# Kernel tuning notes

Measured on AMD Instinct MI355X. Metric: run time of the kernel, lower is better.

## Reference

```python
import jax, jax.numpy as jnp
import numpy as np

WS = 7           # window size (square)
N = WS * WS      # tokens per window = 49
DIM = 384
HEADS = 12
HEAD_DIM = DIM // HEADS
TABLE = (2 * WS - 1) * (2 * WS - 1)  # 169


def _relative_position_index():
    # Static Swin-style relative position index, shape [N, N], values in [0, TABLE)
    coords = np.stack(np.meshgrid(np.arange(WS), np.arange(WS), indexing='ij'))  # [2, WS, WS]
    flat = coords.reshape(2, -1)                           # [2, N]
    rel = flat[:, :, None] - flat[:, None, :]              # [2, N, N]
    rel = rel.transpose(1, 2, 0)                           # [N, N, 2]
    rel[:, :, 0] += WS - 1
    rel[:, :, 1] += WS - 1
    rel[:, :, 0] *= 2 * WS - 1
    return rel.sum(-1)                                     # [N, N]


REL_IDX = jnp.asarray(_relative_position_index())


def setup_inputs() -> dict:
    key = jax.random.key(0)
    ks = jax.random.split(key, 9)
    B_ = 4096
    return {
        'x_edge': jax.random.normal(ks[0], (B_, N, DIM), jnp.float32),
        'x_body': jax.random.normal(ks[1], (B_, N, DIM), jnp.float32),
        'q_w': jax.random.normal(ks[2], (DIM, DIM), jnp.float32) * 0.02,
        'q_b': jnp.zeros((DIM,), jnp.float32),
        'kv_w': jax.random.normal(ks[3], (DIM, 2 * DIM), jnp.float32) * 0.02,
        'kv_b': jnp.zeros((2 * DIM,), jnp.float32),
        'proj_w': jax.random.normal(ks[4], (DIM, DIM), jnp.float32) * 0.02,
        'proj_b': jnp.zeros((DIM,), jnp.float32),
        'bias_table': jax.random.normal(ks[5], (TABLE, HEADS), jnp.float32) * 0.02,
    }


def reference(x_edge, x_body, q_w, q_b, kv_w, kv_b, proj_w, proj_b, bias_table):
    B_, n, C = x_body.shape
    scale = HEAD_DIM ** -0.5
    # projections
    q = (x_edge @ q_w + q_b).reshape(B_, n, HEADS, HEAD_DIM)           # [B,N,H,d]
    kv = (x_body @ kv_w + kv_b).reshape(B_, n, 2, HEADS, HEAD_DIM)
    k = kv[:, :, 0]                                                     # [B,N,H,d]
    v = kv[:, :, 1]
    # windowed attention scores [B,H,N,N]
    attn = jnp.einsum('bnhd,bmhd->bhnm', q * scale, k)
    # gathered relative position bias [H,N,N]
    bias = bias_table[REL_IDX.reshape(-1)].reshape(n, n, HEADS).transpose(2, 0, 1)
    attn = jax.nn.softmax(attn + bias[None], axis=-1)
    out = jnp.einsum('bhnm,bmhd->bnhd', attn, v).reshape(B_, n, C)
    return out @ proj_w + proj_b
```

## Files before the change

kernel.cpp:

```cpp
#include <hip/hip_runtime.h>
#include <hip/hip_bf16.h>

#define NTOK 49
#define DIM 384
#define HEADS 12
#define SCALE 0.17677669529663687f

typedef __attribute__((ext_vector_type(8))) short bf16x8;
typedef __attribute__((ext_vector_type(4))) float f32x4;

#define MFMA16(a, b, c) __builtin_amdgcn_mfma_f32_16x16x32_bf16((a), (b), (c), 0, 0, 0)

__device__ __forceinline__ short f2bf(float f) {
  __hip_bfloat16 h = __float2bfloat16(f);
  return __builtin_bit_cast(short, h);
}

__device__ __forceinline__ bf16x8 pack8(f32x4 a, f32x4 b) {
  bf16x8 r;
#pragma unroll
  for (int i = 0; i < 4; ++i) { r[i] = f2bf(a[i]); r[i + 4] = f2bf(b[i]); }
  return r;
}

#define WQT_OFF   0
#define WKVT_OFF  147456
#define WPT_OFF   442368
#define BIAS_BYTE_OFF 1179648
#define BIAS_ITEMS (12 * 4 * 4 * 64 * 4)

__global__ void prep_kernel(const float* __restrict__ qw, const float* __restrict__ kvw,
                            const float* __restrict__ pw, const float* __restrict__ bt,
                            short* __restrict__ wsS, float* __restrict__ biasf) {
  int id = blockIdx.x * 256 + threadIdx.x;
  const int SZ1 = 384 * 384;
  const int SZ2 = 768 * 384;
  const int SZ3 = 384 * 384;
  if (id < SZ1) {
    int n = id / 384, k = id % 384;
    wsS[WQT_OFF + id] = f2bf(qw[k * 384 + n]);
  } else if (id < SZ1 + SZ2) {
    int t = id - SZ1; int n = t / 384, k = t % 384;
    wsS[WKVT_OFF + t] = f2bf(kvw[k * 768 + n]);
  } else if (id < SZ1 + SZ2 + SZ3) {
    int t = id - (SZ1 + SZ2); int n = t / 384, k = t % 384;
    wsS[WPT_OFF + t] = f2bf(pw[k * 384 + n]);
  } else if (id < SZ1 + SZ2 + SZ3 + BIAS_ITEMS) {
    int t = id - (SZ1 + SZ2 + SZ3);
    int i  = t & 3;
    int lm = (t >> 2) & 63;
    int tb = (t >> 8) & 3;
    int qt = (t >> 10) & 3;
    int h  = t >> 12;
    int q = qt * 16 + (lm & 15);
    int k = tb * 16 + (lm >> 4) * 4 + i;
    float v = 0.0f;
    if (q < NTOK && k < NTOK) {
      int idx = ((q / 7 - k / 7) + 6) * 13 + ((q % 7 - k % 7) + 6);
      v = bt[idx * HEADS + h];
    }
    biasf[t] = v;
  }
}

#define LDS_ELEMS 38416
#define LDS_BYTES (LDS_ELEMS * 2)

__global__ __launch_bounds__(256, 2)
void fused_kernel(const float* __restrict__ xe, const float* __restrict__ xb,
                  const float* __restrict__ qb, const float* __restrict__ kvb,
                  const float* __restrict__ pb,
                  const short* __restrict__ wqT, const short* __restrict__ wkvT,
                  const short* __restrict__ wpT, const float* __restrict__ biasf,
                  float* __restrict__ out) {
  extern __shared__ short lds[];
  short* X    = lds;
  short* XE   = lds + 19208;
  short* OALL = XE;

  const int b   = blockIdx.x;
  const int tid = threadIdx.x;
  const int u   = tid >> 6;
  const int l   = tid & 63;
  const int m16 = l & 15;
  const int g   = l >> 4;

  const f32x4 zf = {0.f, 0.f, 0.f, 0.f};

  const float* xew = xe + (size_t)b * (NTOK * DIM);
  const float* xbw = xb + (size_t)b * (NTOK * DIM);
  for (int i4 = tid; i4 < 2 * 4704; i4 += 256) {
    int eb = i4 < 4704;
    int e = (eb ? i4 : i4 - 4704) * 4;
    const float* src = eb ? xew : xbw;
    short* dst = eb ? XE : X;
    int r = e / DIM, c = e % DIM;
    float4 v = *(const float4*)(src + e);
    ushort4 s;
    s.x = (unsigned short)f2bf(v.x); s.y = (unsigned short)f2bf(v.y);
    s.z = (unsigned short)f2bf(v.z); s.w = (unsigned short)f2bf(v.w);
    *(ushort4*)&dst[r * 392 + c] = s;
  }
  __syncthreads();

  bf16x8 ofr[3][4];

#pragma unroll
  for (int hh = 0; hh < 3; ++hh) {
    const int h = u * 3 + hh;

    f32x4 qc0[4], qc1[4], kc0[4], kc1[4], vc0[4], vc1[4];
#pragma unroll
    for (int tb = 0; tb < 4; ++tb) {
      qc0[tb] = zf; qc1[tb] = zf; kc0[tb] = zf;
      kc1[tb] = zf; vc0[tb] = zf; vc1[tb] = zf;
    }
    const short* wq0 = wqT  + (size_t)(h * 32 + m16) * 384;
    const short* wq1 = wqT  + (size_t)(h * 32 + 16 + m16) * 384;
    const short* wk0 = wkvT + (size_t)(h * 32 + m16) * 384;
    const short* wk1 = wkvT + (size_t)(h * 32 + 16 + m16) * 384;
    const short* wv0 = wkvT + (size_t)(384 + h * 32 + m16) * 384;
    const short* wv1 = wkvT + (size_t)(384 + h * 32 + 16 + m16) * 384;
    bf16x8 qA0 = *(const bf16x8*)(wq0 + g * 8), qA1 = *(const bf16x8*)(wq1 + g * 8);
    bf16x8 kA0 = *(const bf16x8*)(wk0 + g * 8), kA1 = *(const bf16x8*)(wk1 + g * 8);
    bf16x8 vA0 = *(const bf16x8*)(wv0 + g * 8), vA1 = *(const bf16x8*)(wv1 + g * 8);
#pragma unroll 1
    for (int kk = 0; kk < 12; kk += 2) {
      const int koB = (kk + 1) * 32 + g * 8;
      bf16x8 qB0 = *(const bf16x8*)(wq0 + koB), qB1 = *(const bf16x8*)(wq1 + koB);
      bf16x8 kB0 = *(const bf16x8*)(wk0 + koB), kB1 = *(const bf16x8*)(wk1 + koB);
      bf16x8 vB0 = *(const bf16x8*)(wv0 + koB), vB1 = *(const bf16x8*)(wv1 + koB);
      {
        const int ko = kk * 32 + g * 8;
#pragma unroll
        for (int tb = 0; tb < 4; ++tb) {
          int tr = tb * 16 + m16; tr = tr < 49 ? tr : 48;
          bf16x8 xev = *(const bf16x8*)(&XE[tr * 392 + ko]);
          bf16x8 xbv = *(const bf16x8*)(&X[tr * 392 + ko]);
          qc0[tb] = MFMA16(qA0, xev, qc0[tb]);
          qc1[tb] = MFMA16(qA1, xev, qc1[tb]);
          kc0[tb] = MFMA16(kA0, xbv, kc0[tb]);
          kc1[tb] = MFMA16(kA1, xbv, kc1[tb]);
          vc0[tb] = MFMA16(xbv, vA0, vc0[tb]);
          vc1[tb] = MFMA16(xbv, vA1, vc1[tb]);
        }
      }
      const int koA = ((kk + 2) % 12) * 32 + g * 8;
      qA0 = *(const bf16x8*)(wq0 + koA); qA1 = *(const bf16x8*)(wq1 + koA);
      kA0 = *(const bf16x8*)(wk0 + koA); kA1 = *(const bf16x8*)(wk1 + koA);
      vA0 = *(const bf16x8*)(wv0 + koA); vA1 = *(const bf16x8*)(wv1 + koA);
      {
#pragma unroll
        for (int tb = 0; tb < 4; ++tb) {
          int tr = tb * 16 + m16; tr = tr < 49 ? tr : 48;
          bf16x8 xev = *(const bf16x8*)(&XE[tr * 392 + koB]);
          bf16x8 xbv = *(const bf16x8*)(&X[tr * 392 + koB]);
          qc0[tb] = MFMA16(qB0, xev, qc0[tb]);
          qc1[tb] = MFMA16(qB1, xev, qc1[tb]);
          kc0[tb] = MFMA16(kB0, xbv, kc0[tb]);
          kc1[tb] = MFMA16(kB1, xbv, kc1[tb]);
          vc0[tb] = MFMA16(xbv, vB0, vc0[tb]);
          vc1[tb] = MFMA16(xbv, vB1, vc1[tb]);
        }
      }
    }
    bf16x8 qfr[4], kfr[4], vfr[2][2];
    {
      float4 t0 = *(const float4*)(qb + h * 32 + g * 4);
      float4 t1 = *(const float4*)(qb + h * 32 + 16 + g * 4);
      f32x4 b0 = {t0.x, t0.y, t0.z, t0.w};
      f32x4 b1 = {t1.x, t1.y, t1.z, t1.w};
#pragma unroll
      for (int qt = 0; qt < 4; ++qt)
        qfr[qt] = pack8((qc0[qt] + b0) * SCALE, (qc1[qt] + b1) * SCALE);
    }
    {
      float4 t0 = *(const float4*)(kvb + h * 32 + g * 4);
      float4 t1 = *(const float4*)(kvb + h * 32 + 16 + g * 4);
      f32x4 b0 = {t0.x, t0.y, t0.z, t0.w};
      f32x4 b1 = {t1.x, t1.y, t1.z, t1.w};
#pragma unroll
      for (int tb = 0; tb < 4; ++tb) kfr[tb] = pack8(kc0[tb] + b0, kc1[tb] + b1);
    }
    {
      float vb0 = kvb[384 + h * 32 + m16];
      float vb1 = kvb[384 + h * 32 + 16 + m16];
      f32x4 bv0 = {vb0, vb0, vb0, vb0};
      f32x4 bv1 = {vb1, vb1, vb1, vb1};
#pragma unroll
      for (int t = 0; t < 2; ++t) {
        vfr[t][0] = pack8(vc0[2 * t] + bv0, vc0[2 * t + 1] + bv0);
        vfr[t][1] = pack8(vc1[2 * t] + bv1, vc1[2 * t + 1] + bv1);
      }
    }

    const float4* bfh = (const float4*)biasf + (size_t)h * 4 * 4 * 64;
#pragma unroll
    for (int qt = 0; qt < 4; ++qt) {
      const float4* bq = bfh + qt * 4 * 64;
      float4 c0 = bq[l], c1 = bq[64 + l], c2 = bq[128 + l], c3 = bq[192 + l];
      f32x4 B0 = {c0.x, c0.y, c0.z, c0.w};
      f32x4 B1 = {c1.x, c1.y, c1.z, c1.w};
      f32x4 B2 = {c2.x, c2.y, c2.z, c2.w};
      f32x4 B3 = {c3.x, c3.y, c3.z, c3.w};
      f32x4 s[4];
#pragma unroll
      for (int tb = 0; tb < 4; ++tb) s[tb] = MFMA16(kfr[tb], qfr[qt], zf);

      float sv[4][4];
#pragma unroll
      for (int i = 0; i < 4; ++i) {
        sv[0][i] = s[0][i] + B0[i];
        sv[1][i] = s[1][i] + B1[i];
        sv[2][i] = s[2][i] + B2[i];
        sv[3][i] = (g == 0 && i == 0) ? s[3][0] + B3[0] : -3.0e38f;
      }
      float mx = -3.0e38f;
#pragma unroll
      for (int tb = 0; tb < 4; ++tb)
#pragma unroll
        for (int i = 0; i < 4; ++i) mx = fmaxf(mx, sv[tb][i]);
      mx = fmaxf(mx, __shfl_xor(mx, 16));
      mx = fmaxf(mx, __shfl_xor(mx, 32));
      float sum = 0.f;
#pragma unroll
      for (int tb = 0; tb < 4; ++tb)
#pragma unroll
        for (int i = 0; i < 4; ++i) {
          float e = __expf(sv[tb][i] - mx);
          sv[tb][i] = e;
          sum += e;
        }
      sum += __shfl_xor(sum, 16);
      sum += __shfl_xor(sum, 32);
      float inv = 1.0f / sum;

      bf16x8 pfr[2];
#pragma unroll
      for (int t = 0; t < 2; ++t) {
        f32x4 lo = {sv[2 * t][0] * inv, sv[2 * t][1] * inv, sv[2 * t][2] * inv, sv[2 * t][3] * inv};
        f32x4 hi = {sv[2 * t + 1][0] * inv, sv[2 * t + 1][1] * inv, sv[2 * t + 1][2] * inv, sv[2 * t + 1][3] * inv};
        pfr[t] = pack8(lo, hi);
      }
      f32x4 o0 = zf, o1 = zf;
      o0 = MFMA16(pfr[0], vfr[0][0], o0); o0 = MFMA16(pfr[1], vfr[1][0], o0);
      o1 = MFMA16(pfr[0], vfr[0][1], o1); o1 = MFMA16(pfr[1], vfr[1][1], o1);
      ofr[hh][qt] = pack8(o0, o1);
    }
  }
  __syncthreads();

#pragma unroll
  for (int hh = 0; hh < 3; ++hh) {
    const int h = u * 3 + hh;
#pragma unroll
    for (int qt = 0; qt < 4; ++qt)
#pragma unroll
      for (int i = 0; i < 4; ++i) {
        int r = qt * 16 + g * 4 + i;
        if (r < 49) {
          OALL[r * 392 + h * 32 + m16]      = ofr[hh][qt][i];
          OALL[r * 392 + h * 32 + 16 + m16] = ofr[hh][qt][4 + i];
        }
      }
  }
  __syncthreads();

  {
    f32x4 pacc[4][6];
#pragma unroll
    for (int qt = 0; qt < 4; ++qt)
#pragma unroll
      for (int c = 0; c < 6; ++c) pacc[qt][c] = zf;

    const short* wp[6];
    bf16x8 bA[6];
#pragma unroll
    for (int c = 0; c < 6; ++c) {
      wp[c] = wpT + (size_t)((u * 6 + c) * 16 + m16) * 384;
      bA[c] = *(const bf16x8*)(wp[c] + g * 8);
    }
#pragma unroll 1
    for (int kk = 0; kk < 12; kk += 2) {
      const int koB = (kk + 1) * 32 + g * 8;
      bf16x8 bB[6];
#pragma unroll
      for (int c = 0; c < 6; ++c) bB[c] = *(const bf16x8*)(wp[c] + koB);
      {
        const int ko = kk * 32 + g * 8;
        bf16x8 af[4];
#pragma unroll
        for (int qt = 0; qt < 4; ++qt) {
          int r = qt * 16 + m16; r = r < 49 ? r : 48;
          af[qt] = *(const bf16x8*)(&OALL[r * 392 + ko]);
        }
#pragma unroll
        for (int c = 0; c < 6; ++c)
#pragma unroll
          for (int qt = 0; qt < 4; ++qt) pacc[qt][c] = MFMA16(af[qt], bA[c], pacc[qt][c]);
      }
      const int koA = ((kk + 2) % 12) * 32 + g * 8;
#pragma unroll
      for (int c = 0; c < 6; ++c) bA[c] = *(const bf16x8*)(wp[c] + koA);
      {
        bf16x8 af[4];
#pragma unroll
        for (int qt = 0; qt < 4; ++qt) {
          int r = qt * 16 + m16; r = r < 49 ? r : 48;
          af[qt] = *(const bf16x8*)(&OALL[r * 392 + koB]);
        }
#pragma unroll
        for (int c = 0; c < 6; ++c)
#pragma unroll
          for (int qt = 0; qt < 4; ++qt) pacc[qt][c] = MFMA16(af[qt], bB[c], pacc[qt][c]);
      }
    }
    float* outw = out + (size_t)b * (NTOK * DIM);
#pragma unroll
    for (int c = 0; c < 6; ++c) {
      int col = (u * 6 + c) * 16 + m16;
      float pbv = pb[col];
#pragma unroll
      for (int qt = 0; qt < 4; ++qt)
#pragma unroll
        for (int i = 0; i < 4; ++i) {
          int r = qt * 16 + g * 4 + i;
          if (r < 49) outw[r * DIM + col] = pacc[qt][c][i] + pbv;
        }
    }
  }
}

extern "C" void kernel_launch(void* const* d_in, const int* in_sizes, int n_in,
                              void* d_out, int out_size, void* d_ws, size_t ws_size,
                              hipStream_t stream) {
  const float* xe  = (const float*)d_in[0];
  const float* xb  = (const float*)d_in[1];
  const float* qw  = (const float*)d_in[2];
  const float* qb  = (const float*)d_in[3];
  const float* kvw = (const float*)d_in[4];
  const float* kvb = (const float*)d_in[5];
  const float* pw  = (const float*)d_in[6];
  const float* pb  = (const float*)d_in[7];
  const float* bt  = (const float*)d_in[8];
  float* out = (float*)d_out;
  short* wsS = (short*)d_ws;
  float* biasf = (float*)((char*)d_ws + BIAS_BYTE_OFF);

  const int nwin = in_sizes[0] / (NTOK * DIM);

  const int prep_items = 384 * 384 + 768 * 384 + 384 * 384 + BIAS_ITEMS;
  prep_kernel<<<(prep_items + 255) / 256, 256, 0, stream>>>(qw, kvw, pw, bt, wsS, biasf);

  hipFuncSetAttribute((const void*)fused_kernel,
                      hipFuncAttributeMaxDynamicSharedMemorySize, LDS_BYTES);
  fused_kernel<<<nwin, 256, LDS_BYTES, stream>>>(
      xe, xb, qb, kvb, pb,
      wsS + WQT_OFF, wsS + WKVT_OFF, wsS + WPT_OFF, biasf, out);
}
```

Measured before the change: 788.0 us.

## Hoist Q projection for all heads, write attention output directly to LDS

Computes the Q projection for a wave's three heads in one pass before the per-head loop. Each XE fragment is then loaded from LDS once and reused across six MFMA weight tiles, instead of reloading it for every head. Each head's attention output is written straight into the shared LDS buffer, which can overwrite XE once a barrier confirms all Q reads are done. LDS fragments for the K/V and output-projection loops are now software-prefetched one step ahead. The cost is higher register pressure from 24 Q accumulators and prefetch buffers, which may cause spills or lower occupancy under the 2-blocks launch bound.

New measurement: 699.5 us. 11.2% less time.

```diff
diff --git a/kernel.cpp b/kernel.cpp
--- a/kernel.cpp
+++ b/kernel.cpp
@@ -84,11 +84,13 @@
   const int l   = tid & 63;
   const int m16 = l & 15;
   const int g   = l >> 4;
+  const int h0  = u * 3;
 
   const f32x4 zf = {0.f, 0.f, 0.f, 0.f};
 
   const float* xew = xe + (size_t)b * (NTOK * DIM);
   const float* xbw = xb + (size_t)b * (NTOK * DIM);
+#pragma unroll 4
   for (int i4 = tid; i4 < 2 * 4704; i4 += 256) {
     int eb = i4 < 4704;
     int e = (eb ? i4 : i4 - 4704) * 4;
@@ -103,77 +105,118 @@
   }
   __syncthreads();
 
-  bf16x8 ofr[3][4];
+  bf16x8 qfr[3][4];
+  {
+    f32x4 qc[6][4];
+#pragma unroll
+    for (int t = 0; t < 6; ++t)
+#pragma unroll
+      for (int tb = 0; tb < 4; ++tb) qc[t][tb] = zf;
+
+    const short* wq[6];
+    bf16x8 wA[6];
+#pragma unroll
+    for (int t = 0; t < 6; ++t) {
+      wq[t] = wqT + (size_t)((h0 + (t >> 1)) * 32 + (t & 1) * 16 + m16) * 384;
+      wA[t] = *(const bf16x8*)(wq[t] + g * 8);
+    }
+#pragma unroll 1
+    for (int kk = 0; kk < 12; kk += 2) {
+      const int koB = (kk + 1) * 32 + g * 8;
+      bf16x8 wB[6];
+#pragma unroll
+      for (int t = 0; t < 6; ++t) wB[t] = *(const bf16x8*)(wq[t] + koB);
+      {
+        const int ko = kk * 32 + g * 8;
+#pragma unroll
+        for (int tb = 0; tb < 4; ++tb) {
+          int tr = tb * 16 + m16; tr = tr < 49 ? tr : 48;
+          bf16x8 xv = *(const bf16x8*)(&XE[tr * 392 + ko]);
+#pragma unroll
+          for (int t = 0; t < 6; ++t) qc[t][tb] = MFMA16(wA[t], xv, qc[t][tb]);
+        }
+      }
+      const int koA = ((kk + 2) % 12) * 32 + g * 8;
+#pragma unroll
+      for (int t = 0; t < 6; ++t) wA[t] = *(const bf16x8*)(wq[t] + koA);
+      {
+#pragma unroll
+        for (int tb = 0; tb < 4; ++tb) {
+          int tr = tb * 16 + m16; tr = tr < 49 ? tr : 48;
+          bf16x8 xv = *(const bf16x8*)(&XE[tr * 392 + koB]);
+#pragma unroll
+          for (int t = 0; t < 6; ++t) qc[t][tb] = MFMA16(wB[t], xv, qc[t][tb]);
+        }
+      }
+    }
+#pragma unroll
+    for (int hh = 0; hh < 3; ++hh) {
+      const int h = h0 + hh;
+      float4 t0 = *(const float4*)(qb + h * 32 + g * 4);
+      float4 t1 = *(const float4*)(qb + h * 32 + 16 + g * 4);
+      f32x4 b0 = {t0.x, t0.y, t0.z, t0.w};
+      f32x4 b1 = {t1.x, t1.y, t1.z, t1.w};
+#pragma unroll
+      for (int qt = 0; qt < 4; ++qt)
+        qfr[hh][qt] = pack8((qc[hh * 2][qt] + b0) * SCALE, (qc[hh * 2 + 1][qt] + b1) * SCALE);
+    }
+  }
+  __syncthreads();
 
 #pragma unroll
   for (int hh = 0; hh < 3; ++hh) {
-    const int h = u * 3 + hh;
-
-    f32x4 qc0[4], qc1[4], kc0[4], kc1[4], vc0[4], vc1[4];
-#pragma unroll
-    for (int tb = 0; tb < 4; ++tb) {
-      qc0[tb] = zf; qc1[tb] = zf; kc0[tb] = zf;
-      kc1[tb] = zf; vc0[tb] = zf; vc1[tb] = zf;
-    }
-    const short* wq0 = wqT  + (size_t)(h * 32 + m16) * 384;
-    const short* wq1 = wqT  + (size_t)(h * 32 + 16 + m16) * 384;
+    const int h = h0 + hh;
+
+    f32x4 kc0[4], kc1[4], vc0[4], vc1[4];
+#pragma unroll
+    for (int tb = 0; tb < 4; ++tb) { kc0[tb] = zf; kc1[tb] = zf; vc0[tb] = zf; vc1[tb] = zf; }
     const short* wk0 = wkvT + (size_t)(h * 32 + m16) * 384;
     const short* wk1 = wkvT + (size_t)(h * 32 + 16 + m16) * 384;
     const short* wv0 = wkvT + (size_t)(384 + h * 32 + m16) * 384;
     const short* wv1 = wkvT + (size_t)(384 + h * 32 + 16 + m16) * 384;
-    bf16x8 qA0 = *(const bf16x8*)(wq0 + g * 8), qA1 = *(const bf16x8*)(wq1 + g * 8);
     bf16x8 kA0 = *(const bf16x8*)(wk0 + g * 8), kA1 = *(const bf16x8*)(wk1 + g * 8);
     bf16x8 vA0 = *(const bf16x8*)(wv0 + g * 8), vA1 = *(const bf16x8*)(wv1 + g * 8);
+    bf16x8 xbA[4];
+#pragma unroll
+    for (int tb = 0; tb < 4; ++tb) {
+      int tr = tb * 16 + m16; tr = tr < 49 ? tr : 48;
+      xbA[tb] = *(const bf16x8*)(&X[tr * 392 + g * 8]);
+    }
 #pragma unroll 1
     for (int kk = 0; kk < 12; kk += 2) {
       const int koB = (kk + 1) * 32 + g * 8;
-      bf16x8 qB0 = *(const bf16x8*)(wq0 + koB), qB1 = *(const bf16x8*)(wq1 + koB);
       bf16x8 kB0 = *(const bf16x8*)(wk0 + koB), kB1 = *(const bf16x8*)(wk1 + koB);
       bf16x8 vB0 = *(const bf16x8*)(wv0 + koB), vB1 = *(const bf16x8*)(wv1 + koB);
-      {
-        const int ko = kk * 32 + g * 8;
-#pragma unroll
-        for (int tb = 0; tb < 4; ++tb) {
-          int tr = tb * 16 + m16; tr = tr < 49 ? tr : 48;
-          bf16x8 xev = *(const bf16x8*)(&XE[tr * 392 + ko]);
-          bf16x8 xbv = *(const bf16x8*)(&X[tr * 392 + ko]);
-          qc0[tb] = MFMA16(qA0, xev, qc0[tb]);
-          qc1[tb] = MFMA16(qA1, xev, qc1[tb]);
-          kc0[tb] = MFMA16(kA0, xbv, kc0[tb]);
-          kc1[tb] = MFMA16(kA1, xbv, kc1[tb]);
-          vc0[tb] = MFMA16(xbv, vA0, vc0[tb]);
-          vc1[tb] = MFMA16(xbv, vA1, vc1[tb]);
-        }
+      bf16x8 xbB[4];
+#pragma unroll
+      for (int tb = 0; tb < 4; ++tb) {
+        int tr = tb * 16 + m16; tr = tr < 49 ? tr : 48;
+        xbB[tb] = *(const bf16x8*)(&X[tr * 392 + koB]);
+      }
+#pragma unroll
+      for (int tb = 0; tb < 4; ++tb) {
+        kc0[tb] = MFMA16(kA0, xbA[tb], kc0[tb]);
+        kc1[tb] = MFMA16(kA1, xbA[tb], kc1[tb]);
+        vc0[tb] = MFMA16(xbA[tb], vA0, vc0[tb]);
+        vc1[tb] = MFMA16(xbA[tb], vA1, vc1[tb]);
       }
       const int koA = ((kk + 2) % 12) * 32 + g * 8;
-      qA0 = *(const bf16x8*)(wq0 + koA); qA1 = *(const bf16x8*)(wq1 + koA);
       kA0 = *(const bf16x8*)(wk0 + koA); kA1 = *(const bf16x8*)(wk1 + koA);
       vA0 = *(const bf16x8*)(wv0 + koA); vA1 = *(const bf16x8*)(wv1 + koA);
-      {
-#pragma unroll
-        for (int tb = 0; tb < 4; ++tb) {
-          int tr = tb * 16 + m16; tr = tr < 49 ? tr : 48;
-          bf16x8 xev = *(const bf16x8*)(&XE[tr * 392 + koB]);
-          bf16x8 xbv = *(const bf16x8*)(&X[tr * 392 + koB]);
-          qc0[tb] = MFMA16(qB0, xev, qc0[tb]);
-          qc1[tb] = MFMA16(qB1, xev, qc1[tb]);
-          kc0[tb] = MFMA16(kB0, xbv, kc0[tb]);
-          kc1[tb] = MFMA16(kB1, xbv, kc1[tb]);
-          vc0[tb] = MFMA16(xbv, vB0, vc0[tb]);
-          vc1[tb] = MFMA16(xbv, vB1, vc1[tb]);
-        }
-      }
-    }
-    bf16x8 qfr[4], kfr[4], vfr[2][2];
-    {
-      float4 t0 = *(const float4*)(qb + h * 32 + g * 4);
-      float4 t1 = *(const float4*)(qb + h * 32 + 16 + g * 4);
-      f32x4 b0 = {t0.x, t0.y, t0.z, t0.w};
-      f32x4 b1 = {t1.x, t1.y, t1.z, t1.w};
-#pragma unroll
-      for (int qt = 0; qt < 4; ++qt)
-        qfr[qt] = pack8((qc0[qt] + b0) * SCALE, (qc1[qt] + b1) * SCALE);
-    }
+#pragma unroll
+      for (int tb = 0; tb < 4; ++tb) {
+        int tr = tb * 16 + m16; tr = tr < 49 ? tr : 48;
+        xbA[tb] = *(const bf16x8*)(&X[tr * 392 + koA]);
+      }
+#pragma unroll
+      for (int tb = 0; tb < 4; ++tb) {
+        kc0[tb] = MFMA16(kB0, xbB[tb], kc0[tb]);
+        kc1[tb] = MFMA16(kB1, xbB[tb], kc1[tb]);
+        vc0[tb] = MFMA16(xbB[tb], vB0, vc0[tb]);
+        vc1[tb] = MFMA16(xbB[tb], vB1, vc1[tb]);
+      }
+    }
+    bf16x8 kfr[4], vfr[2][2];
     {
       float4 t0 = *(const float4*)(kvb + h * 32 + g * 4);
       float4 t1 = *(const float4*)(kvb + h * 32 + 16 + g * 4);
@@ -205,7 +248,7 @@
       f32x4 B3 = {c3.x, c3.y, c3.z, c3.w};
       f32x4 s[4];
 #pragma unroll
-      for (int tb = 0; tb < 4; ++tb) s[tb] = MFMA16(kfr[tb], qfr[qt], zf);
+      for (int tb = 0; tb < 4; ++tb) s[tb] = MFMA16(kfr[tb], qfr[hh][qt], zf);
 
       float sv[4][4];
 #pragma unroll
@@ -245,24 +288,15 @@
       f32x4 o0 = zf, o1 = zf;
       o0 = MFMA16(pfr[0], vfr[0][0], o0); o0 = MFMA16(pfr[1], vfr[1][0], o0);
       o1 = MFMA16(pfr[0], vfr[0][1], o1); o1 = MFMA16(pfr[1], vfr[1][1], o1);
-      ofr[hh][qt] = pack8(o0, o1);
-    }
-  }
-  __syncthreads();
-
-#pragma unroll
-  for (int hh = 0; hh < 3; ++hh) {
-    const int h = u * 3 + hh;
-#pragma unroll
-    for (int qt = 0; qt < 4; ++qt)
 #pragma unroll
       for (int i = 0; i < 4; ++i) {
         int r = qt * 16 + g * 4 + i;
         if (r < 49) {
-          OALL[r * 392 + h * 32 + m16]      = ofr[hh][qt][i];
-          OALL[r * 392 + h * 32 + 16 + m16] = ofr[hh][qt][4 + i];
-        }
-      }
+          OALL[r * 392 + h * 32 + m16]      = f2bf(o0[i]);
+          OALL[r * 392 + h * 32 + 16 + m16] = f2bf(o1[i]);
+        }
+      }
+    }
   }
   __syncthreads();
 
@@ -273,6 +307,11 @@
 #pragma unroll
       for (int c = 0; c < 6; ++c) pacc[qt][c] = zf;
 
+    int rq[4];
+#pragma unroll
+    for (int qt = 0; qt < 4; ++qt) {
+      int r = qt * 16 + m16; rq[qt] = r < 49 ? r : 48;
+    }
     const short* wp[6];
     bf16x8 bA[6];
 #pragma unroll
@@ -280,40 +319,31 @@
       wp[c] = wpT + (size_t)((u * 6 + c) * 16 + m16) * 384;
       bA[c] = *(const bf16x8*)(wp[c] + g * 8);
     }
+    bf16x8 afA[4];
+#pragma unroll
+    for (int qt = 0; qt < 4; ++qt) afA[qt] = *(const bf16x8*)(&OALL[rq[qt] * 392 + g * 8]);
 #pragma unroll 1
     for (int kk = 0; kk < 12; kk += 2) {
       const int koB = (kk + 1) * 32 + g * 8;
       bf16x8 bB[6];
 #pragma unroll
       for (int c = 0; c < 6; ++c) bB[c] = *(const bf16x8*)(wp[c] + koB);
-      {
-        const int ko = kk * 32 + g * 8;
-        bf16x8 af[4];
-#pragma unroll
-        for (int qt = 0; qt < 4; ++qt) {
-          int r = qt * 16 + m16; r = r < 49 ? r : 48;
-          af[qt] = *(const bf16x8*)(&OALL[r * 392 + ko]);
-        }
-#pragma unroll
-        for (int c = 0; c < 6; ++c)
-#pragma unroll
-          for (int qt = 0; qt < 4; ++qt) pacc[qt][c] = MFMA16(af[qt], bA[c], pacc[qt][c]);
-      }
+      bf16x8 afB[4];
+#pragma unroll
+      for (int qt = 0; qt < 4; ++qt) afB[qt] = *(const bf16x8*)(&OALL[rq[qt] * 392 + koB]);
+#pragma unroll
+      for (int c = 0; c < 6; ++c)
+#pragma unroll
+        for (int qt = 0; qt < 4; ++qt) pacc[qt][c] = MFMA16(afA[qt], bA[c], pacc[qt][c]);
       const int koA = ((kk + 2) % 12) * 32 + g * 8;
 #pragma unroll
       for (int c = 0; c < 6; ++c) bA[c] = *(const bf16x8*)(wp[c] + koA);
-      {
-        bf16x8 af[4];
-#pragma unroll
-        for (int qt = 0; qt < 4; ++qt) {
-          int r = qt * 16 + m16; r = r < 49 ? r : 48;
-          af[qt] = *(const bf16x8*)(&OALL[r * 392 + koB]);
-        }
-#pragma unroll
-        for (int c = 0; c < 6; ++c)
-#pragma unroll
-          for (int qt = 0; qt < 4; ++qt) pacc[qt][c] = MFMA16(af[qt], bB[c], pacc[qt][c]);
-      }
+#pragma unroll
+      for (int qt = 0; qt < 4; ++qt) afA[qt] = *(const bf16x8*)(&OALL[rq[qt] * 392 + koA]);
+#pragma unroll
+      for (int c = 0; c < 6; ++c)
+#pragma unroll
+        for (int qt = 0; qt < 4; ++qt) pacc[qt][c] = MFMA16(afB[qt], bB[c], pacc[qt][c]);
     }
     float* outw = out + (size_t)b * (NTOK * DIM);
 #pragma unroll
```
